# Kernel optimization log

Hardware: AMD Instinct MI355X
Metric: run time of the kernel (lower is better)

Reference implementation:

```python
import jax, jax.numpy as jnp
import numpy as np

N_NODES = 80000
N_EDGES = 1280000
NODE_DIM = 32
EDGE_DIM = 16
HIDDEN = 64
N_HIDDEN_LAYERS = 3  # layer_count - 1
NUM_GRAPHS = 256


def setup_inputs() -> dict:
    key = jax.random.key(0)
    ks = jax.random.split(key, 16)
    s = 0.05
    H = jax.random.normal(ks[0], (N_NODES, NODE_DIM), dtype=jnp.float32)
    Xe = jax.random.normal(ks[1], (N_EDGES, EDGE_DIM), dtype=jnp.float32)
    id_Xe = jax.random.randint(ks[2], (2, N_EDGES), 0, N_NODES, dtype=jnp.int32).astype(jnp.int64)
    batch_idx = jnp.sort(jax.random.randint(ks[3], (N_NODES,), 0, NUM_GRAPHS, dtype=jnp.int32)).astype(jnp.int64)
    # input layer: M: (node+edge)->hidden, U: (hidden+node)->hidden
    Mw0 = jax.random.normal(ks[4], (NODE_DIM + EDGE_DIM, HIDDEN), dtype=jnp.float32) * s
    Mb0 = jnp.zeros((HIDDEN,), dtype=jnp.float32)
    Uw0 = jax.random.normal(ks[5], (HIDDEN + NODE_DIM, HIDDEN), dtype=jnp.float32) * s
    Ub0 = jnp.zeros((HIDDEN,), dtype=jnp.float32)
    # hidden layers: M: (hidden+edge)->hidden, U: (2*hidden)->hidden (stacked)
    Mw_h = jax.random.normal(ks[6], (N_HIDDEN_LAYERS, HIDDEN + EDGE_DIM, HIDDEN), dtype=jnp.float32) * s
    Mb_h = jnp.zeros((N_HIDDEN_LAYERS, HIDDEN), dtype=jnp.float32)
    Uw_h = jax.random.normal(ks[7], (N_HIDDEN_LAYERS, 2 * HIDDEN, HIDDEN), dtype=jnp.float32) * s
    Ub_h = jnp.zeros((N_HIDDEN_LAYERS, HIDDEN), dtype=jnp.float32)
    # final linear head hidden -> 1
    Ww = jax.random.normal(ks[8], (HIDDEN, 1), dtype=jnp.float32) * s
    Wb = jnp.zeros((1,), dtype=jnp.float32)
    return {"H": H, "Xe": Xe, "id_Xe": id_Xe, "batch_idx": batch_idx,
            "Mw0": Mw0, "Mb0": Mb0, "Uw0": Uw0, "Ub0": Ub0,
            "Mw_h": Mw_h, "Mb_h": Mb_h, "Uw_h": Uw_h, "Ub_h": Ub_h,
            "Ww": Ww, "Wb": Wb}


def reference(H, Xe, id_Xe, batch_idx, Mw0, Mb0, Uw0, Ub0, Mw_h, Mb_h, Uw_h, Ub_h, Ww, Wb):
    n = H.shape[0]
    src = id_Xe[0]
    dst = id_Xe[1]

    def gnn_layer(h, Mw, Mb, Uw, Ub):
        # message: gather source node features, concat edge features, MLP M
        m = jax.nn.relu(jnp.concatenate([h[src], Xe], axis=-1) @ Mw + Mb)  # [E, hidden]
        # scatter-sum to target nodes
        agg = jax.ops.segment_sum(m, dst, num_segments=n)  # [N, hidden]
        # update: concat node state with aggregated message, MLP U
        return jax.nn.relu(jnp.concatenate([h, agg], axis=-1) @ Uw + Ub)

    y = gnn_layer(H, Mw0, Mb0, Uw0, Ub0)
    for i in range(Mw_h.shape[0]):
        y = gnn_layer(y, Mw_h[i], Mb_h[i], Uw_h[i], Ub_h[i])

    pooled = jax.ops.segment_sum(y, batch_idx, num_segments=NUM_GRAPHS)  # [G, hidden]
    return pooled @ Ww + Wb  # [G, 1]
```

## Files before the change

kernel.cpp:

```cpp
#include <hip/hip_runtime.h>
#include <hip/hip_fp16.h>

#define HID 64

struct alignas(8)  H4 { __half2 a, b; };
struct alignas(16) H8 { __half2 h[4]; };

typedef _Float16 f16x8 __attribute__((ext_vector_type(8)));
typedef float    f32x4 __attribute__((ext_vector_type(4)));

__global__ __launch_bounds__(256) void deg_count(const int* __restrict__ dst,
                                                 int* __restrict__ deg, int E) {
    int e = blockIdx.x * 256 + threadIdx.x;
    if (e < E) atomicAdd(&deg[dst[e]], 1);
}

__global__ __launch_bounds__(256) void scan1(const int* __restrict__ deg,
                                             int* __restrict__ rowptr,
                                             int* __restrict__ bsums, int N) {
    __shared__ int s[256];
    const int t = threadIdx.x;
    const int base = blockIdx.x * 2048 + t * 8;
    int v[8], tot = 0;
    #pragma unroll
    for (int i = 0; i < 8; i++) {
        int x = (base + i < N) ? deg[base + i] : 0;
        v[i] = tot; tot += x;
    }
    s[t] = tot; __syncthreads();
    for (int off = 1; off < 256; off <<= 1) {
        int a = (t >= off) ? s[t - off] : 0;
        __syncthreads(); s[t] += a; __syncthreads();
    }
    const int texcl = s[t] - tot;
    #pragma unroll
    for (int i = 0; i < 8; i++)
        if (base + i < N) rowptr[base + i] = texcl + v[i];
    if (t == 255) bsums[blockIdx.x] = s[255];
}

__global__ void scan2(int* bsums, int NB) {
    if (blockIdx.x == 0 && threadIdx.x == 0) {
        int run = 0;
        for (int i = 0; i < NB; i++) { int x = bsums[i]; bsums[i] = run; run += x; }
    }
}

__global__ __launch_bounds__(256) void scan3(int* __restrict__ rowptr,
                                             const int* __restrict__ bsums,
                                             int N, int E) {
    int idx = blockIdx.x * 256 + threadIdx.x;
    if (idx < N) rowptr[idx] += bsums[idx >> 11];
    if (idx == 0) rowptr[N] = E;
}

__global__ __launch_bounds__(256) void permute_k(
    const int* __restrict__ src, const int* __restrict__ dst,
    const int* __restrict__ rowptr, int* __restrict__ cursor,
    const float* __restrict__ Xe, __half* __restrict__ Xes,
    unsigned* __restrict__ pks, int E)
{
    int e = blockIdx.x * 256 + threadIdx.x;
    if (e >= E) return;
    int d = dst[e];
    int pos = rowptr[d] + atomicAdd(&cursor[d], 1);
    pks[pos] = ((unsigned)src[e] << 5) | (unsigned)(d & 31);
    const float4* xi = (const float4*)&Xe[(size_t)e * 16];
    float4 x0 = xi[0], x1 = xi[1], x2 = xi[2], x3 = xi[3];
    H8 h0, h1;
    h0.h[0] = __float22half2_rn(make_float2(x0.x, x0.y));
    h0.h[1] = __float22half2_rn(make_float2(x0.z, x0.w));
    h0.h[2] = __float22half2_rn(make_float2(x1.x, x1.y));
    h0.h[3] = __float22half2_rn(make_float2(x1.z, x1.w));
    h1.h[0] = __float22half2_rn(make_float2(x2.x, x2.y));
    h1.h[1] = __float22half2_rn(make_float2(x2.z, x2.w));
    h1.h[2] = __float22half2_rn(make_float2(x3.x, x3.y));
    h1.h[3] = __float22half2_rn(make_float2(x3.z, x3.w));
    H8* xo = (H8*)&Xes[(size_t)pos * 16];
    xo[0] = h0; xo[1] = h1;
}

template<int K1>
__global__ __launch_bounds__(256) void pm_dual(
    const float* __restrict__ Hn,
    const float* __restrict__ Wm, const float* __restrict__ bm,
    const float* __restrict__ Wu, const float* __restrict__ bu,
    __half* __restrict__ PMh, __half* __restrict__ Th, int N)
{
    constexpr int KP = K1 + 4;
    constexpr int P4 = K1 / 4;
    __shared__ float Ws[K1 * 128];
    __shared__ float Xs[32 * KP];

    const int tid = threadIdx.x;
    for (int i = tid; i < K1 * 32; i += 256) {
        const int row = i >> 5, c4 = i & 31;
        float4 v = (c4 < 16) ? *(const float4*)&Wm[row * 64 + c4 * 4]
                             : *(const float4*)&Wu[row * 64 + (c4 - 16) * 4];
        *(float4*)&Ws[row * 128 + c4 * 4] = v;
    }
    const int nbase = blockIdx.x * 32;
    for (int i = tid; i < 32 * P4; i += 256) {
        const int nl = i / P4, part = i % P4;
        const int n = nbase + nl;
        if (n < N)
            *(float4*)&Xs[nl * KP + part * 4] =
                *(const float4*)&Hn[(size_t)n * K1 + part * 4];
    }
    __syncthreads();

    const int c0 = (tid & 31) * 4;
    const int n0 = (tid >> 5) * 4;
    const float4 bv = (c0 < 64) ? *(const float4*)&bm[c0]
                                : *(const float4*)&bu[c0 - 64];

    float4 acc[4];
    #pragma unroll
    for (int i = 0; i < 4; i++) acc[i] = bv;

    #pragma unroll 4
    for (int k = 0; k < K1; k += 4) {
        const float4 w0 = *(const float4*)&Ws[(k + 0) * 128 + c0];
        const float4 w1 = *(const float4*)&Ws[(k + 1) * 128 + c0];
        const float4 w2 = *(const float4*)&Ws[(k + 2) * 128 + c0];
        const float4 w3 = *(const float4*)&Ws[(k + 3) * 128 + c0];
        #pragma unroll
        for (int ni = 0; ni < 4; ni++) {
            const float4 xv = *(const float4*)&Xs[(n0 + ni) * KP + k];
            acc[ni].x += xv.x * w0.x + xv.y * w1.x + xv.z * w2.x + xv.w * w3.x;
            acc[ni].y += xv.x * w0.y + xv.y * w1.y + xv.z * w2.y + xv.w * w3.y;
            acc[ni].z += xv.x * w0.z + xv.y * w1.z + xv.z * w2.z + xv.w * w3.z;
            acc[ni].w += xv.x * w0.w + xv.y * w1.w + xv.z * w2.w + xv.w * w3.w;
        }
    }

    #pragma unroll
    for (int ni = 0; ni < 4; ni++) {
        const int n = nbase + n0 + ni;
        if (n < N) {
            H4 o;
            o.a = __float22half2_rn(make_float2(acc[ni].x, acc[ni].y));
            o.b = __float22half2_rn(make_float2(acc[ni].z, acc[ni].w));
            if (c0 < 64) *(H4*)&PMh[(size_t)n * 64 + c0]      = o;
            else         *(H4*)&Th [(size_t)n * 64 + c0 - 64] = o;
        }
    }
}

__global__ __launch_bounds__(256) void edge_fused(
    const __half*   __restrict__ PMh,
    const __half*   __restrict__ Th,
    const __half*   __restrict__ Xes,
    const unsigned* __restrict__ pks,
    const int*      __restrict__ rowptr,
    const float*    __restrict__ Mwb,
    const float*    __restrict__ Uwb,
    float*          __restrict__ Yout,
    int N)
{
    constexpr int AGP = HID + 4;
    __shared__ float aggs[32 * AGP];

    const int tid  = threadIdx.x;
    const int wv   = tid >> 6;
    const int lane = tid & 63;
    const int n    = lane & 15;
    const int quad = lane >> 4;

    f16x8 bfrag[4];
    #pragma unroll
    for (int s = 0; s < 4; s++) {
        f16x8 b;
        #pragma unroll
        for (int jj = 0; jj < 8; jj++) {
            const int k = quad * 8 + jj;
            float w = (k < 16) ? Mwb[k * 64 + 16 * s + n]
                               : ((k - 16) == n ? 1.f : 0.f);
            b[jj] = (_Float16)w;
        }
        bfrag[s] = b;
    }

    for (int i = tid; i < 32 * AGP; i += 256) aggs[i] = 0.f;

    const int nbase  = blockIdx.x * 32;
    const int nend   = (nbase + 32 < N) ? nbase + 32 : N;
    const int estart = rowptr[nbase];
    const int eend   = rowptr[nend];
    __syncthreads();

    int pc = estart + wv * 16;
    unsigned spk_c = 0, spk_n = 0, spk_n2 = 0;
    f16x8 af_c[4], af_n[4];

    auto loadA = [&](int p0, unsigned spk, f16x8* af) {
        const __half* xbase = Xes + (size_t)(p0 + n) * 16 + quad * 8;
        const __half* pbase = PMh + (size_t)(spk >> 5) * 64 + (quad - 2) * 8;
        #pragma unroll
        for (int s = 0; s < 4; s++) {
            const __half* p = (quad < 2) ? xbase : (pbase + 16 * s);
            af[s] = *(const f16x8*)p;
        }
    };

    if (pc < eend) {
        {
            const int pe = pc + n;
            spk_c = pks[pe < eend ? pe : eend - 1];
        }
        if (pc + 64 < eend) {
            const int pe = pc + 64 + n;
            spk_n = pks[pe < eend ? pe : eend - 1];
        }
        loadA(pc, spk_c, af_c);
    }

    for (; pc < eend; pc += 64) {
        const int pn  = pc + 64;
        const int pn2 = pc + 128;

        if (pn < eend) loadA(pn, spk_n, af_n);
        if (pn2 < eend) {
            const int pe = pn2 + n;
            spk_n2 = pks[pe < eend ? pe : eend - 1];
        }

        int qld[4];
        #pragma unroll
        for (int r = 0; r < 4; r++)
            qld[r] = (int)(__shfl(spk_c, quad * 4 + r) & 31u);

        f32x4 acc[4];
        #pragma unroll
        for (int s = 0; s < 4; s++)
            acc[s] = __builtin_amdgcn_mfma_f32_16x16x32_f16(
                af_c[s], bfrag[s], (f32x4){0.f, 0.f, 0.f, 0.f}, 0, 0, 0);

        int ldp = -1;
        float rs0 = 0.f, rs1 = 0.f, rs2 = 0.f, rs3 = 0.f;
        #pragma unroll
        for (int r = 0; r < 4; r++) {
            const bool valid = (pc + quad * 4 + r) < eend;
            const int ld = valid ? qld[r] : -1;
            const float v0 = fmaxf(acc[0][r], 0.f);
            const float v1 = fmaxf(acc[1][r], 0.f);
            const float v2 = fmaxf(acc[2][r], 0.f);
            const float v3 = fmaxf(acc[3][r], 0.f);
            if (ld == ldp) {
                rs0 += v0; rs1 += v1; rs2 += v2; rs3 += v3;
            } else {
                if (ldp >= 0) {
                    float* a = &aggs[ldp * AGP + n];
                    atomicAdd(a +  0, rs0); atomicAdd(a + 16, rs1);
                    atomicAdd(a + 32, rs2); atomicAdd(a + 48, rs3);
                }
                rs0 = v0; rs1 = v1; rs2 = v2; rs3 = v3; ldp = ld;
            }
        }
        if (ldp >= 0) {
            float* a = &aggs[ldp * AGP + n];
            atomicAdd(a +  0, rs0); atomicAdd(a + 16, rs1);
            atomicAdd(a + 32, rs2); atomicAdd(a + 48, rs3);
        }

        spk_c = spk_n; spk_n = spk_n2;
        #pragma unroll
        for (int s = 0; s < 4; s++) af_c[s] = af_n[s];
    }

    __syncthreads();

    {
        const int c0t = (tid & 15) * 4;
        const int r0  = tid >> 4;
        const int r1  = r0 + 16;
        const int n0g = nbase + r0, n1g = nbase + r1;
        float4 acc0 = make_float4(0.f, 0.f, 0.f, 0.f);
        float4 acc1 = make_float4(0.f, 0.f, 0.f, 0.f);
        if (n0g < N) {
            H4 th = *(const H4*)&Th[(size_t)n0g * 64 + c0t];
            float2 lo = __half22float2(th.a), hi = __half22float2(th.b);
            acc0 = make_float4(lo.x, lo.y, hi.x, hi.y);
        }
        if (n1g < N) {
            H4 th = *(const H4*)&Th[(size_t)n1g * 64 + c0t];
            float2 lo = __half22float2(th.a), hi = __half22float2(th.b);
            acc1 = make_float4(lo.x, lo.y, hi.x, hi.y);
        }
        #pragma unroll 4
        for (int k = 0; k < 64; k += 4) {
            const float4 w0 = *(const float4*)&Uwb[(k + 0) * 64 + c0t];
            const float4 w1 = *(const float4*)&Uwb[(k + 1) * 64 + c0t];
            const float4 w2 = *(const float4*)&Uwb[(k + 2) * 64 + c0t];
            const float4 w3 = *(const float4*)&Uwb[(k + 3) * 64 + c0t];
            const float4 x0 = *(const float4*)&aggs[r0 * AGP + k];
            const float4 x1 = *(const float4*)&aggs[r1 * AGP + k];
            acc0.x += x0.x * w0.x + x0.y * w1.x + x0.z * w2.x + x0.w * w3.x;
            acc0.y += x0.x * w0.y + x0.y * w1.y + x0.z * w2.y + x0.w * w3.y;
            acc0.z += x0.x * w0.z + x0.y * w1.z + x0.z * w2.z + x0.w * w3.z;
            acc0.w += x0.x * w0.w + x0.y * w1.w + x0.z * w2.w + x0.w * w3.w;
            acc1.x += x1.x * w0.x + x1.y * w1.x + x1.z * w2.x + x1.w * w3.x;
            acc1.y += x1.x * w0.y + x1.y * w1.y + x1.z * w2.y + x1.w * w3.y;
            acc1.z += x1.x * w0.z + x1.y * w1.z + x1.z * w2.z + x1.w * w3.z;
            acc1.w += x1.x * w0.w + x1.y * w1.w + x1.z * w2.w + x1.w * w3.w;
        }
        if (n0g < N) {
            float4 o;
            o.x = fmaxf(acc0.x, 0.f); o.y = fmaxf(acc0.y, 0.f);
            o.z = fmaxf(acc0.z, 0.f); o.w = fmaxf(acc0.w, 0.f);
            *(float4*)&Yout[(size_t)n0g * HID + c0t] = o;
        }
        if (n1g < N) {
            float4 o;
            o.x = fmaxf(acc1.x, 0.f); o.y = fmaxf(acc1.y, 0.f);
            o.z = fmaxf(acc1.z, 0.f); o.w = fmaxf(acc1.w, 0.f);
            *(float4*)&Yout[(size_t)n1g * HID + c0t] = o;
        }
    }
}

__global__ __launch_bounds__(256) void pool_head(
    const float* __restrict__ Y, const int* __restrict__ bidx,
    const float* __restrict__ Ww, const float* __restrict__ Wb,
    float* __restrict__ out, int N)
{
    const int g = blockIdx.x;
    int a = 0, b = N;
    while (a < b) { int m = (a + b) >> 1; if (bidx[m] < g) a = m + 1; else b = m; }
    const int lo = a;
    b = N;
    while (a < b) { int m = (a + b) >> 1; if (bidx[m] < g + 1) a = m + 1; else b = m; }
    const int hi = a;

    const int tid = threadIdx.x;
    const int c4 = tid & 15, nl = tid >> 4;
    float4 s = make_float4(0.f, 0.f, 0.f, 0.f);
    for (int n = lo + nl; n < hi; n += 16) {
        const float4 v = *(const float4*)&Y[(size_t)n * HID + c4 * 4];
        s.x += v.x; s.y += v.y; s.z += v.z; s.w += v.w;
    }
    __shared__ float red[16 * 68];
    *(float4*)&red[nl * 68 + c4 * 4] = s;
    __syncthreads();
    if (tid < 64) {
        float t = 0.f;
        #pragma unroll
        for (int r = 0; r < 16; r++) t += red[r * 68 + tid];
        t *= Ww[tid];
        #pragma unroll
        for (int off = 32; off; off >>= 1) t += __shfl_down(t, off);
        if (tid == 0) out[g] = t + Wb[0];
    }
}

extern "C" void kernel_launch(void* const* d_in, const int* in_sizes, int n_in,
                              void* d_out, int out_size, void* d_ws, size_t ws_size,
                              hipStream_t stream) {
    const float* H    = (const float*)d_in[0];
    const float* Xe   = (const float*)d_in[1];
    const int*   ids  = (const int*)d_in[2];
    const int*   bidx = (const int*)d_in[3];
    const float* Mw0  = (const float*)d_in[4];
    const float* Mb0  = (const float*)d_in[5];
    const float* Uw0  = (const float*)d_in[6];
    const float* Ub0  = (const float*)d_in[7];
    const float* MwH  = (const float*)d_in[8];
    const float* MbH  = (const float*)d_in[9];
    const float* UwH  = (const float*)d_in[10];
    const float* UbH  = (const float*)d_in[11];
    const float* Ww   = (const float*)d_in[12];
    const float* Wb   = (const float*)d_in[13];
    float* out = (float*)d_out;

    const int N = in_sizes[0] / 32;
    const int E = in_sizes[1] / 16;
    const int* src = ids;
    const int* dst = ids + E;

    float*  hbuf = (float*)d_ws;
    __half* PMh  = (__half*)(hbuf + (size_t)N * HID);
    __half* Th   = PMh + (size_t)N * HID;
    __half* Xes  = Th  + (size_t)N * HID;
    unsigned* pks = (unsigned*)(Xes + (size_t)E * 16);
    int* rowptr  = (int*)(pks + E);
    int* deg     = rowptr + (N + 1);
    int* bsums   = deg + N;

    const int NB = (N + 2047) / 2048;
    const int eblocks = (E + 255) / 256;
    const int ntile   = (N + 31) / 32;

    hipMemsetAsync(deg, 0, (size_t)N * sizeof(int), stream);
    deg_count<<<eblocks, 256, 0, stream>>>(dst, deg, E);
    scan1<<<NB, 256, 0, stream>>>(deg, rowptr, bsums, N);
    scan2<<<1, 64, 0, stream>>>(bsums, NB);
    scan3<<<(N + 255) / 256, 256, 0, stream>>>(rowptr, bsums, N, E);
    hipMemsetAsync(deg, 0, (size_t)N * sizeof(int), stream);
    permute_k<<<eblocks, 256, 0, stream>>>(src, dst, rowptr, deg,
                                           Xe, Xes, pks, E);

    pm_dual<32><<<ntile, 256, 0, stream>>>(H, Mw0, Mb0, Uw0, Ub0, PMh, Th, N);
    edge_fused<<<ntile, 256, 0, stream>>>(PMh, Th, Xes, pks, rowptr,
                                          Mw0 + 32 * HID, Uw0 + 32 * HID, hbuf, N);

    for (int l = 0; l < 3; l++) {
        const float* Mw = MwH + (size_t)l * 80 * HID;
        const float* Uw = UwH + (size_t)l * 128 * HID;
        pm_dual<64><<<ntile, 256, 0, stream>>>(hbuf, Mw, MbH + (size_t)l * HID,
                                               Uw, UbH + (size_t)l * HID, PMh, Th, N);
        edge_fused<<<ntile, 256, 0, stream>>>(PMh, Th, Xes, pks, rowptr,
                                              Mw + 64 * HID, Uw + 64 * HID, hbuf, N);
    }

    pool_head<<<256, 256, 0, stream>>>(hbuf, bidx, Ww, Wb, out, N);
}
```

Before: 972.5 us.

## Process 32 edges per wave iteration with double-buffered A-fragment prefetch

Each wave in the fused edge kernel now handles two 16-edge groups per loop step (stride 128 per block instead of 64), loading packed indices for 32 edges at once and swapping them across half-waves with a shuffle. This doubles the loads in flight and the MFMA work per iteration, which is meant to hide gather latency and amortize loop overhead. It costs twice the register space for prefetched fragments, which may lower occupancy, and gives coarser load balancing at the edge-range tail.

```diff
diff --git a/kernel.cpp b/kernel.cpp
--- a/kernel.cpp
+++ b/kernel.cpp
@@ -161,11 +161,13 @@
     constexpr int AGP = HID + 4;
     __shared__ float aggs[32 * AGP];
 
-    const int tid  = threadIdx.x;
-    const int wv   = tid >> 6;
-    const int lane = tid & 63;
-    const int n    = lane & 15;
-    const int quad = lane >> 4;
+    const int tid   = threadIdx.x;
+    const int wv    = tid >> 6;
+    const int lane  = tid & 63;
+    const int n     = lane & 15;
+    const int quad  = lane >> 4;
+    const int l31   = lane & 31;
+    const bool ownG1 = (lane >> 4) & 1;
 
     f16x8 bfrag[4];
     #pragma unroll
@@ -189,83 +191,95 @@
     const int eend   = rowptr[nend];
     __syncthreads();
 
-    int pc = estart + wv * 16;
+    auto loadPK = [&](int p) -> unsigned {
+        const int pe = p + l31;
+        return pks[pe < eend ? pe : eend - 1];
+    };
+    auto loadA32 = [&](int p, unsigned spk, f16x8 af[2][4]) {
+        const unsigned spk_x = (unsigned)__shfl((int)spk, lane ^ 16);
+        const unsigned sg0 = ownG1 ? spk_x : spk;
+        const unsigned sg1 = ownG1 ? spk : spk_x;
+        #pragma unroll
+        for (int g2 = 0; g2 < 2; g2++) {
+            int ei = p + g2 * 16 + n;
+            ei = ei < eend ? ei : eend - 1;
+            const __half* xb = Xes + (size_t)ei * 16 + quad * 8;
+            const unsigned sgv = g2 ? sg1 : sg0;
+            const __half* pb = PMh + (size_t)(sgv >> 5) * 64 + (quad - 2) * 8;
+            #pragma unroll
+            for (int s = 0; s < 4; s++) {
+                const __half* ptr = (quad < 2) ? xb : (pb + 16 * s);
+                af[g2][s] = *(const f16x8*)ptr;
+            }
+        }
+    };
+
+    int pc = estart + wv * 32;
     unsigned spk_c = 0, spk_n = 0, spk_n2 = 0;
-    f16x8 af_c[4], af_n[4];
-
-    auto loadA = [&](int p0, unsigned spk, f16x8* af) {
-        const __half* xbase = Xes + (size_t)(p0 + n) * 16 + quad * 8;
-        const __half* pbase = PMh + (size_t)(spk >> 5) * 64 + (quad - 2) * 8;
-        #pragma unroll
-        for (int s = 0; s < 4; s++) {
-            const __half* p = (quad < 2) ? xbase : (pbase + 16 * s);
-            af[s] = *(const f16x8*)p;
-        }
-    };
+    f16x8 af_c[2][4], af_n[2][4];
 
     if (pc < eend) {
-        {
-            const int pe = pc + n;
-            spk_c = pks[pe < eend ? pe : eend - 1];
-        }
-        if (pc + 64 < eend) {
-            const int pe = pc + 64 + n;
-            spk_n = pks[pe < eend ? pe : eend - 1];
-        }
-        loadA(pc, spk_c, af_c);
-    }
-
-    for (; pc < eend; pc += 64) {
-        const int pn  = pc + 64;
-        const int pn2 = pc + 128;
-
-        if (pn < eend) loadA(pn, spk_n, af_n);
-        if (pn2 < eend) {
-            const int pe = pn2 + n;
-            spk_n2 = pks[pe < eend ? pe : eend - 1];
-        }
-
-        int qld[4];
-        #pragma unroll
-        for (int r = 0; r < 4; r++)
-            qld[r] = (int)(__shfl(spk_c, quad * 4 + r) & 31u);
-
-        f32x4 acc[4];
-        #pragma unroll
-        for (int s = 0; s < 4; s++)
-            acc[s] = __builtin_amdgcn_mfma_f32_16x16x32_f16(
-                af_c[s], bfrag[s], (f32x4){0.f, 0.f, 0.f, 0.f}, 0, 0, 0);
-
-        int ldp = -1;
-        float rs0 = 0.f, rs1 = 0.f, rs2 = 0.f, rs3 = 0.f;
-        #pragma unroll
-        for (int r = 0; r < 4; r++) {
-            const bool valid = (pc + quad * 4 + r) < eend;
-            const int ld = valid ? qld[r] : -1;
-            const float v0 = fmaxf(acc[0][r], 0.f);
-            const float v1 = fmaxf(acc[1][r], 0.f);
-            const float v2 = fmaxf(acc[2][r], 0.f);
-            const float v3 = fmaxf(acc[3][r], 0.f);
-            if (ld == ldp) {
-                rs0 += v0; rs1 += v1; rs2 += v2; rs3 += v3;
-            } else {
-                if (ldp >= 0) {
-                    float* a = &aggs[ldp * AGP + n];
-                    atomicAdd(a +  0, rs0); atomicAdd(a + 16, rs1);
-                    atomicAdd(a + 32, rs2); atomicAdd(a + 48, rs3);
+        spk_c = loadPK(pc);
+        if (pc + 128 < eend) spk_n = loadPK(pc + 128);
+        loadA32(pc, spk_c, af_c);
+    }
+
+    for (; pc < eend; pc += 128) {
+        const int pn  = pc + 128;
+        const int pn2 = pc + 256;
+
+        if (pn < eend)  loadA32(pn, spk_n, af_n);
+        if (pn2 < eend) spk_n2 = loadPK(pn2);
+
+        #pragma unroll
+        for (int g2 = 0; g2 < 2; g2++) {
+            const int gbase = pc + g2 * 16;
+
+            int qld[4];
+            #pragma unroll
+            for (int r = 0; r < 4; r++)
+                qld[r] = (int)((unsigned)__shfl((int)spk_c,
+                               g2 * 16 + quad * 4 + r) & 31u);
+
+            f32x4 acc[4];
+            #pragma unroll
+            for (int s = 0; s < 4; s++)
+                acc[s] = __builtin_amdgcn_mfma_f32_16x16x32_f16(
+                    af_c[g2][s], bfrag[s], (f32x4){0.f, 0.f, 0.f, 0.f}, 0, 0, 0);
+
+            int ldp = -1;
+            float rs0 = 0.f, rs1 = 0.f, rs2 = 0.f, rs3 = 0.f;
+            #pragma unroll
+            for (int r = 0; r < 4; r++) {
+                const bool valid = (gbase + quad * 4 + r) < eend;
+                const int ld = valid ? qld[r] : -1;
+                const float v0 = fmaxf(acc[0][r], 0.f);
+                const float v1 = fmaxf(acc[1][r], 0.f);
+                const float v2 = fmaxf(acc[2][r], 0.f);
+                const float v3 = fmaxf(acc[3][r], 0.f);
+                if (ld == ldp) {
+                    rs0 += v0; rs1 += v1; rs2 += v2; rs3 += v3;
+                } else {
+                    if (ldp >= 0) {
+                        float* a = &aggs[ldp * AGP + n];
+                        atomicAdd(a +  0, rs0); atomicAdd(a + 16, rs1);
+                        atomicAdd(a + 32, rs2); atomicAdd(a + 48, rs3);
+                    }
+                    rs0 = v0; rs1 = v1; rs2 = v2; rs3 = v3; ldp = ld;
                 }
-                rs0 = v0; rs1 = v1; rs2 = v2; rs3 = v3; ldp = ld;
             }
-        }
-        if (ldp >= 0) {
-            float* a = &aggs[ldp * AGP + n];
-            atomicAdd(a +  0, rs0); atomicAdd(a + 16, rs1);
-            atomicAdd(a + 32, rs2); atomicAdd(a + 48, rs3);
+            if (ldp >= 0) {
+                float* a = &aggs[ldp * AGP + n];
+                atomicAdd(a +  0, rs0); atomicAdd(a + 16, rs1);
+                atomicAdd(a + 32, rs2); atomicAdd(a + 48, rs3);
+            }
         }
 
         spk_c = spk_n; spk_n = spk_n2;
         #pragma unroll
-        for (int s = 0; s < 4; s++) af_c[s] = af_n[s];
+        for (int g2 = 0; g2 < 2; g2++)
+            #pragma unroll
+            for (int s = 0; s < 4; s++) af_c[g2][s] = af_n[g2][s];
     }
 
     __syncthreads();
```

Measured after the change: 983.6 us. About the same (+1.1%).
